# Kernel optimization log

Hardware: AMD Instinct MI355X
Metric: run time of the kernel (lower is better)

## Reference

```python
import jax, jax.numpy as jnp
import numpy as np

B, S, D, H = 2, 2048, 2048, 16
HD = D // H
RESIDUAL_SCALE = 1.0
EPS = 1e-6


def setup_inputs() -> dict:
    key = jax.random.key(0)
    ks = jax.random.split(key, 6)
    x = jax.random.normal(ks[0], (B, S, D), jnp.float32)
    # rotary tables: emb = cat(freqs, freqs), shape [S, HD]
    inv_freq = 1.0 / (10000.0 ** (jnp.arange(0, HD, 2, dtype=jnp.float32) / HD))
    t = jnp.arange(S, dtype=jnp.float32)
    freqs = jnp.einsum('s,f->sf', t, inv_freq)
    emb = jnp.concatenate([freqs, freqs], axis=-1)
    cos, sin = jnp.cos(emb), jnp.sin(emb)
    sc = 0.02
    w_qkv = jax.random.normal(ks[1], (3 * D, D), jnp.float32) * sc
    w_out = jax.random.normal(ks[2], (D, D), jnp.float32) * sc
    w_fc1 = jax.random.normal(ks[3], (4 * D, D), jnp.float32) * sc
    w_fc2 = jax.random.normal(ks[4], (D, 4 * D), jnp.float32) * sc
    g1 = jnp.ones((D,), jnp.float32)
    g2 = jnp.ones((D,), jnp.float32)
    return {'x': x, 'cos': cos, 'sin': sin, 'g1': g1, 'g2': g2,
            'w_qkv': w_qkv, 'w_out': w_out, 'w_fc1': w_fc1, 'w_fc2': w_fc2}


def _rmsnorm(x, g):
    xf = x.astype(jnp.float32)
    norm = jnp.sqrt(jnp.mean(xf * xf, axis=-1, keepdims=True) + EPS)
    return g * (xf / norm)


def _rotate_half(x):
    x1, x2 = jnp.split(x, 2, axis=-1)
    return jnp.concatenate([-x2, x1], axis=-1)


def _rope(t, cos, sin):
    # t: [B, S, H, HD]; cos/sin: [S, HD]
    c = cos[None, :, None, :]
    s = sin[None, :, None, :]
    return t * c + _rotate_half(t) * s


def reference(x, cos, sin, g1, g2, w_qkv, w_out, w_fc1, w_fc2):
    b, s, d = x.shape
    x_skip = x
    h = _rmsnorm(x, g1)
    qkv = (h @ w_qkv.T).reshape(b, s, 3, H, HD)
    q = _rope(qkv[:, :, 0], cos, sin)
    k = _rope(qkv[:, :, 1], cos, sin)
    v = qkv[:, :, 2]  # rotary is identity on v
    scale = 1.0 / jnp.sqrt(jnp.asarray(HD, dtype=q.dtype))
    scores = jnp.einsum('bqhd,bkhd->bhqk', q, k) * scale
    causal = jnp.triu(jnp.ones((s, s), dtype=bool), k=1)
    scores = jnp.where(causal[None, None], -jnp.inf, scores)
    attn = jax.nn.softmax(scores, axis=-1)
    o = jnp.einsum('bhqk,bkhd->bqhd', attn, v).reshape(b, s, d)
    x = x_skip + RESIDUAL_SCALE * (o @ w_out.T)
    x_skip = x
    h = _rmsnorm(x, g2)
    h = jax.nn.gelu(h @ w_fc1.T, approximate=True) @ w_fc2.T
    return x_skip + RESIDUAL_SCALE * h
```

## Files before the change

kernel.cpp:

```cpp
#include <hip/hip_runtime.h>
#include <stdint.h>

typedef unsigned short u16;
typedef u16 u16x4 __attribute__((ext_vector_type(4)));
typedef u16 u16x8 __attribute__((ext_vector_type(8)));
typedef __bf16 bf16x8 __attribute__((ext_vector_type(8)));
typedef float f32x4 __attribute__((ext_vector_type(4)));
typedef float f32x16 __attribute__((ext_vector_type(16)));

#define MFMA16 __builtin_amdgcn_mfma_f32_16x16x32_bf16
#define MFMA32 __builtin_amdgcn_mfma_f32_32x32x16_bf16

static __device__ __forceinline__ float b2f(u16 u) {
    union { unsigned int i; float f; } v; v.i = ((unsigned int)u) << 16; return v.f;
}
static __device__ __forceinline__ u16 f2b(float f) {
    union { float f; unsigned int i; } v; v.f = f;
    unsigned int r = (v.i + 0x7fffu + ((v.i >> 16) & 1u)) >> 16;
    return (u16)r;
}
static __device__ __forceinline__ unsigned pk2(float lo, float hi) {
    union { __bf16 b[2]; unsigned u; } t;
    t.b[0] = (__bf16)lo; t.b[1] = (__bf16)hi; return t.u;
}
static __device__ __forceinline__ void gload_lds16(const void* g, void* l) {
    __builtin_amdgcn_global_load_lds((__attribute__((address_space(1))) void*)g,
                                     (__attribute__((address_space(3))) void*)l,
                                     16, 0, 0);
}

__global__ __launch_bounds__(256) void cvt_k(const float* __restrict__ in,
                                             u16* __restrict__ out, long n) {
    long i = ((long)blockIdx.x * 256 + threadIdx.x) * 4;
    if (i >= n) return;
    float4 v = *(const float4*)(in + i);
    u16x4 o; o[0] = f2b(v.x); o[1] = f2b(v.y); o[2] = f2b(v.z); o[3] = f2b(v.w);
    *(u16x4*)(out + i) = o;
}

__global__ __launch_bounds__(256) void addred_k(float* __restrict__ xout,
                                                const float* __restrict__ p0,
                                                const float* __restrict__ p1) {
    long i = ((long)blockIdx.x * 256 + threadIdx.x) * 4;
    float4 a = *(const float4*)(xout + i);
    float4 b = *(const float4*)(p0 + i);
    float4 c = *(const float4*)(p1 + i);
    a.x += b.x + c.x; a.y += b.y + c.y; a.z += b.z + c.z; a.w += b.w + c.w;
    *(float4*)(xout + i) = a;
}

__global__ __launch_bounds__(256) void addrednorm_k(float* xout,
                                                    const float* __restrict__ x,
                                                    const float* p0,
                                                    const float* __restrict__ p1,
                                                    const float* __restrict__ g,
                                                    u16* __restrict__ out) {
    const long row = blockIdx.x;
    const int tid = threadIdx.x;
    const long base = row * 2048;
    float4 a = *(const float4*)(x + base + tid * 4);
    float4 b = *(const float4*)(p0 + base + tid * 4);
    float4 c = *(const float4*)(p1 + base + tid * 4);
    a.x += b.x + c.x; a.y += b.y + c.y; a.z += b.z + c.z; a.w += b.w + c.w;
    float4 a2 = *(const float4*)(x + base + 1024 + tid * 4);
    float4 b2 = *(const float4*)(p0 + base + 1024 + tid * 4);
    float4 c2 = *(const float4*)(p1 + base + 1024 + tid * 4);
    a2.x += b2.x + c2.x; a2.y += b2.y + c2.y;
    a2.z += b2.z + c2.z; a2.w += b2.w + c2.w;
    *(float4*)(xout + base + tid * 4) = a;
    *(float4*)(xout + base + 1024 + tid * 4) = a2;
    float ss = a.x*a.x + a.y*a.y + a.z*a.z + a.w*a.w
             + a2.x*a2.x + a2.y*a2.y + a2.z*a2.z + a2.w*a2.w;
    #pragma unroll
    for (int d = 1; d < 64; d <<= 1) ss += __shfl_xor(ss, d);
    __shared__ float red[4];
    if ((tid & 63) == 0) red[tid >> 6] = ss;
    __syncthreads();
    float tot = red[0] + red[1] + red[2] + red[3];
    float rinv = rsqrtf(tot * (1.0f / 2048.0f) + 1e-6f);
    float4 g0 = *(const float4*)(g + tid * 4);
    float4 g1 = *(const float4*)(g + 1024 + tid * 4);
    u16x4 o0, o1;
    o0[0] = f2b(a.x * g0.x * rinv); o0[1] = f2b(a.y * g0.y * rinv);
    o0[2] = f2b(a.z * g0.z * rinv); o0[3] = f2b(a.w * g0.w * rinv);
    o1[0] = f2b(a2.x * g1.x * rinv); o1[1] = f2b(a2.y * g1.y * rinv);
    o1[2] = f2b(a2.z * g1.z * rinv); o1[3] = f2b(a2.w * g1.w * rinv);
    *(u16x4*)(out + base + tid * 4) = o0;
    *(u16x4*)(out + base + 1024 + tid * 4) = o1;
}

__global__ __launch_bounds__(256) void rmsnorm_k(const float* __restrict__ x,
                                                 const float* __restrict__ g,
                                                 u16* __restrict__ out) {
    const long row = blockIdx.x;
    const int tid = threadIdx.x;
    const float* xr = x + row * 2048;
    float4 a = *(const float4*)(xr + tid * 4);
    float4 b = *(const float4*)(xr + 1024 + tid * 4);
    float ss = a.x*a.x + a.y*a.y + a.z*a.z + a.w*a.w
             + b.x*b.x + b.y*b.y + b.z*b.z + b.w*b.w;
    #pragma unroll
    for (int d = 1; d < 64; d <<= 1) ss += __shfl_xor(ss, d);
    __shared__ float red[4];
    if ((tid & 63) == 0) red[tid >> 6] = ss;
    __syncthreads();
    float tot = red[0] + red[1] + red[2] + red[3];
    float rinv = rsqrtf(tot * (1.0f / 2048.0f) + 1e-6f);
    float4 g0 = *(const float4*)(g + tid * 4);
    float4 g1 = *(const float4*)(g + 1024 + tid * 4);
    u16x4 o0, o1;
    o0[0] = f2b(a.x * g0.x * rinv); o0[1] = f2b(a.y * g0.y * rinv);
    o0[2] = f2b(a.z * g0.z * rinv); o0[3] = f2b(a.w * g0.w * rinv);
    o1[0] = f2b(b.x * g1.x * rinv); o1[1] = f2b(b.y * g1.y * rinv);
    o1[2] = f2b(b.z * g1.z * rinv); o1[3] = f2b(b.w * g1.w * rinv);
    *(u16x4*)(out + row * 2048 + tid * 4) = o0;
    *(u16x4*)(out + row * 2048 + 1024 + tid * 4) = o1;
}

__global__ __launch_bounds__(256) void rope_k(u16* __restrict__ qkv,
                                              const float* __restrict__ cosb,
                                              const float* __restrict__ sinb) {
    long idx = (long)blockIdx.x * 256 + threadIdx.x;
    int d = (int)(idx & 15) * 4;
    int h = (int)((idx >> 4) & 15);
    int which = (int)((idx >> 8) & 1);
    long row = idx >> 9;
    int s = (int)(row & 2047);
    u16* base = qkv + row * 6144 + which * 2048 + h * 128;
    u16x4 ua = *(u16x4*)(base + d);
    u16x4 ub = *(u16x4*)(base + d + 64);
    float4 c4 = *(const float4*)(cosb + (long)s * 128 + d);
    float4 s4 = *(const float4*)(sinb + (long)s * 128 + d);
    float cc[4] = {c4.x, c4.y, c4.z, c4.w};
    float sn[4] = {s4.x, s4.y, s4.z, s4.w};
    float scale = (which == 0) ? 0.08838834764831845f : 1.0f;
    u16x4 oa, ob;
    #pragma unroll
    for (int j = 0; j < 4; ++j) {
        float a = b2f(ua[j]), b = b2f(ub[j]);
        oa[j] = f2b((a * cc[j] - b * sn[j]) * scale);
        ob[j] = f2b((b * cc[j] + a * sn[j]) * scale);
    }
    *(u16x4*)(base + d) = oa;
    *(u16x4*)(base + d + 64) = ob;
}

#define DS_A(BUF, SM, KK) (*(const bf16x8*)(ldsb + (BUF)*32768 + \
        ((((SM)*2) + (KK)) << 10) + rin64 + cst2))
#define DS_B(BUF, SN, KK) (*(const bf16x8*)(ldsb + 65536 + (BUF)*32768 + \
        ((((SN)*2) + (KK)) << 10) + rin64 + cst2))
#define STAGE_AB(BUF, SK, KT) do { \
    gload_lds16(sA0 + ((long)(KT)*64 + (SK)*32), ldsb + (BUF)*32768 + (w4 + (SK))*1024); \
    gload_lds16(sA1 + ((long)(KT)*64 + (SK)*32), ldsb + (BUF)*32768 + (w4 + 2 + (SK))*1024); \
    gload_lds16(sB0 + ((long)(KT)*64 + (SK)*32), ldsb + 65536 + (BUF)*32768 + (w4 + (SK))*1024); \
    gload_lds16(sB1 + ((long)(KT)*64 + (SK)*32), ldsb + 65536 + (BUF)*32768 + (w4 + 2 + (SK))*1024); \
} while (0)
#define PHASE(BUF, MH, KK, RDB, STAGE_STMT, VM) do { \
    bf16x8 af[4]; \
    _Pragma("unroll") \
    for (int m = 0; m < 4; ++m) af[m] = DS_A(BUF, wr8 + (MH)*4 + m, KK); \
    if (RDB) { \
        bfr[0] = DS_B(BUF, wc4 + 0, KK); bfr[1] = DS_B(BUF, wc4 + 1, KK); \
        bfr[2] = DS_B(BUF, wc4 + 2, KK); bfr[3] = DS_B(BUF, wc4 + 3, KK); \
    } \
    STAGE_STMT; \
    if (VM) { asm volatile("s_waitcnt vmcnt(8)" ::: "memory"); } \
    __builtin_amdgcn_sched_barrier(0); \
    __builtin_amdgcn_s_barrier(); \
    __builtin_amdgcn_sched_barrier(0); \
    __builtin_amdgcn_s_setprio(1); \
    _Pragma("unroll") \
    for (int m = 0; m < 4; ++m) \
        _Pragma("unroll") \
        for (int n = 0; n < 4; ++n) \
            acc[(MH)*4 + m][n] = MFMA16(af[m], bfr[n], acc[(MH)*4 + m][n], 0, 0, 0); \
    __builtin_amdgcn_s_setprio(0); \
    __builtin_amdgcn_sched_barrier(0); \
    __builtin_amdgcn_s_barrier(); \
    __builtin_amdgcn_sched_barrier(0); \
} while (0)

template <int EPI>
__global__ __launch_bounds__(512, 2) void gemm256(const u16* __restrict__ A,
                                                  const u16* __restrict__ W,
                                                  int M, int N, int K,
                                                  u16* outb, float* outf,
                                                  float* outf2, const float* res,
                                                  u16* vtw, int ksplit) {
    __shared__ u16 lds_[65536];
    char* ldsb = (char*)lds_;
    const int tid = threadIdx.x;
    const int w = tid >> 6, l = tid & 63;
    const int w4 = w * 4;
    const int wr8 = (w >> 2) * 8;
    const int wc4 = (w & 3) * 4;
    const int rin64 = (l & 15) * 64;
    const int cst2 = ((((l >> 4) * 8) ^ (((l >> 3) & 1) << 4)) << 1);

    const int nbn = N >> 8;
    const int nbm = M >> 8;
    const int nwg = gridDim.x;
    const int cpx = nwg >> 3;
    const int bid = blockIdx.x;
    int wg = (bid & 7) * cpx + (bid >> 3);
    int kseg = 0;
    int Keff = K;
    if (ksplit == 2) {
        kseg = wg & 1;
        wg >>= 1;
        Keff = K >> 1;
    }
    const int grp = 8 * nbn;
    const int g8 = wg / grp;
    const int rem = wg - g8 * grp;
    const int bm0 = g8 * 8;
    const int gmh = (nbm - bm0 < 8) ? (nbm - bm0) : 8;
    const int bn = rem / gmh;
    const int bm = bm0 + rem % gmh;
    const u16* Ab = A + (long)kseg * Keff;
    const u16* Wb = W + (long)kseg * Keff;

    const int r4 = l >> 2;
    const int clog = ((l & 3) * 8) ^ (((r4 >> 3) & 1) << 4);
    const u16* sA0 = Ab + ((long)bm * 256 + (w * 2 + 0) * 16 + r4) * K + clog;
    const u16* sA1 = Ab + ((long)bm * 256 + (w * 2 + 1) * 16 + r4) * K + clog;
    const u16* sB0 = Wb + ((long)bn * 256 + (w * 2 + 0) * 16 + r4) * K + clog;
    const u16* sB1 = Wb + ((long)bn * 256 + (w * 2 + 1) * 16 + r4) * K + clog;

    f32x4 acc[8][4];
    #pragma unroll
    for (int m = 0; m < 8; ++m)
        #pragma unroll
        for (int n = 0; n < 4; ++n) acc[m][n] = (f32x4){0.f, 0.f, 0.f, 0.f};
    bf16x8 bfr[4];

    const int nkt = Keff >> 6;
    const int niter = nkt >> 1;

    STAGE_AB(0, 0, 0); STAGE_AB(0, 1, 0); STAGE_AB(1, 0, 1);
    asm volatile("s_waitcnt vmcnt(8)" ::: "memory");
    __builtin_amdgcn_sched_barrier(0);
    __builtin_amdgcn_s_barrier();
    __builtin_amdgcn_sched_barrier(0);

    for (int it = 0; it < niter; ++it) {
        const int t = it * 2;
        const int t1 = t + 1;
        const int t2 = (t + 2 < nkt) ? t + 2 : nkt - 1;
        const int t3 = (t + 3 < nkt) ? t + 3 : nkt - 1;
        PHASE(0, 0, 0, 1, STAGE_AB(1, 1, t1), 0);
        PHASE(0, 1, 0, 0, ;, 1);
        PHASE(0, 0, 1, 1, STAGE_AB(0, 0, t2), 0);
        PHASE(0, 1, 1, 0, ;, 1);
        PHASE(1, 0, 0, 1, STAGE_AB(0, 1, t2), 0);
        PHASE(1, 1, 0, 0, ;, 1);
        PHASE(1, 0, 1, 1, STAGE_AB(1, 0, t3), 0);
        PHASE(1, 1, 1, 0, ;, 1);
    }
    asm volatile("s_waitcnt vmcnt(0)" ::: "memory");

    const int rb = bm * 256 + (wr8 >> 3) * 128 + ((l >> 4) << 2);
    const int cb = bn * 256 + (w & 3) * 64 + (l & 15);
    if (EPI == 4) {
        const bool vreg = (cb >= 4096);
        #pragma unroll
        for (int m = 0; m < 8; ++m) {
            long row0 = rb + m * 16;
            #pragma unroll
            for (int n = 0; n < 4; ++n) {
                long col = cb + n * 16;
                if (vreg) {
                    int d = (int)col & 127;
                    int hh = ((int)col >> 7) - 32;
                    long bh = (row0 >> 11) * 16 + hh;
                    int s = (int)(row0 & 2047);
                    u16x4 o4;
                    #pragma unroll
                    for (int r = 0; r < 4; ++r) o4[r] = f2b(acc[m][n][r]);
                    *(u16x4*)(vtw + (bh * 128 + d) * 2048 + s) = o4;
                } else {
                    #pragma unroll
                    for (int r = 0; r < 4; ++r)
                        outb[(row0 + r) * N + col] = f2b(acc[m][n][r]);
                }
            }
        }
        return;
    }
    float* pf = (EPI == 3) ? (kseg ? outf2 : outf) : outf;
    #pragma unroll
    for (int m = 0; m < 8; ++m) {
        #pragma unroll
        for (int r = 0; r < 4; ++r) {
            long row = rb + m * 16 + r;
            #pragma unroll
            for (int n = 0; n < 4; ++n) {
                long col = cb + n * 16;
                float v = acc[m][n][r];
                if (EPI == 1) {
                    pf[row * N + col] = res[row * N + col] + v;
                } else if (EPI == 2) {
                    float u = 0.7978845608028654f * v * (1.0f + 0.044715f * v * v);
                    float e = __expf(2.0f * u);
                    float tgl = 1.0f - 2.0f / (e + 1.0f);
                    outb[row * N + col] = f2b(0.5f * v * (1.0f + tgl));
                } else if (EPI == 3) {
                    pf[row * N + col] = v;
                } else {
                    outb[row * N + col] = f2b(v);
                }
            }
        }
    }
}

struct AttnState {
    f32x16 acc[4];
    float m_i, l_i;
};

template <bool DIAG>
static __device__ __forceinline__ void attn_tile(
    int kv0, int qg, bool do_g1, int l31, int hi,
    const u16* __restrict__ Ks, const u16* __restrict__ Vt,
    const bf16x8 (&qf)[8], AttnState& st)
{
    f32x16 sacc0, sacc1;
    #pragma unroll
    for (int r = 0; r < 16; ++r) { sacc0[r] = 0.f; sacc1[r] = 0.f; }

    #pragma unroll
    for (int dsl = 0; dsl < 8; ++dsl) {
        int slot = dsl * 2 + hi;
        int kv = l31;
        int sw = (slot & 8) | ((slot & 7) ^ (kv & 7));
        bf16x8 kf = *(const bf16x8*)(Ks + kv * 128 + sw * 8);
        sacc0 = MFMA32(kf, qf[dsl], sacc0, 0, 0, 0);
    }
    if (do_g1) {
        #pragma unroll
        for (int dsl = 0; dsl < 8; ++dsl) {
            int slot = dsl * 2 + hi;
            int kv = 32 + l31;
            int sw = (slot & 8) | ((slot & 7) ^ (kv & 7));
            bf16x8 kf = *(const bf16x8*)(Ks + kv * 128 + sw * 8);
            sacc1 = MFMA32(kf, qf[dsl], sacc1, 0, 0, 0);
        }
    }

    float sv[2][16];
    #pragma unroll
    for (int r = 0; r < 16; ++r) {
        sv[0][r] = sacc0[r];
        sv[1][r] = do_g1 ? sacc1[r] : -INFINITY;
    }
    if (DIAG) {
        #pragma unroll
        for (int g = 0; g < 2; ++g)
            #pragma unroll
            for (int r = 0; r < 16; ++r) {
                int kvg = kv0 + g * 32 + ((r & 3) + 8 * (r >> 2) + 4 * hi);
                if (kvg > qg) sv[g][r] = -INFINITY;
            }
    }

    float mx = sv[0][0];
    #pragma unroll
    for (int r = 1; r < 16; ++r) mx = fmaxf(mx, sv[0][r]);
    #pragma unroll
    for (int r = 0; r < 16; ++r) mx = fmaxf(mx, sv[1][r]);
    mx = fmaxf(mx, __shfl_xor(mx, 32));

    bool defer = __all(mx <= st.m_i + 8.0f);
    if (!defer) {
        float mnew = fmaxf(st.m_i, mx);
        float f = __expf(st.m_i - mnew);
        st.l_i *= f;
        #pragma unroll
        for (int dblk = 0; dblk < 4; ++dblk)
            #pragma unroll
            for (int r = 0; r < 16; ++r) st.acc[dblk][r] *= f;
        st.m_i = mnew;
    }

    float ssum = 0.f;
    #pragma unroll
    for (int g = 0; g < 2; ++g)
        #pragma unroll
        for (int r = 0; r < 16; ++r) {
            float e = __expf(sv[g][r] - st.m_i);
            sv[g][r] = e;
            ssum += e;
        }
    ssum += __shfl_xor(ssum, 32);
    st.l_i += ssum;

    unsigned w[2][4][2];
    #pragma unroll
    for (int g = 0; g < 2; ++g)
        #pragma unroll
        for (int q4 = 0; q4 < 4; ++q4) {
            w[g][q4][0] = pk2(sv[g][4 * q4 + 0], sv[g][4 * q4 + 1]);
            w[g][q4][1] = pk2(sv[g][4 * q4 + 2], sv[g][4 * q4 + 3]);
        }
    bf16x8 pfrag[4];
    #pragma unroll
    for (int ks = 0; ks < 4; ++ks) {
        int g = ks >> 1, h2 = ks & 1;
        unsigned o0 = hi ? w[g][2 * h2 + 1][0] : w[g][2 * h2][0];
        unsigned o1 = hi ? w[g][2 * h2 + 1][1] : w[g][2 * h2][1];
        unsigned t0 = hi ? w[g][2 * h2][0] : w[g][2 * h2 + 1][0];
        unsigned t1 = hi ? w[g][2 * h2][1] : w[g][2 * h2 + 1][1];
        unsigned s0v = __shfl_xor(t0, 32);
        unsigned s1v = __shfl_xor(t1, 32);
        union { unsigned u[4]; bf16x8 v; } cv;
        cv.u[0] = hi ? s0v : o0;
        cv.u[1] = hi ? s1v : o1;
        cv.u[2] = hi ? o0 : s0v;
        cv.u[3] = hi ? o1 : s1v;
        pfrag[ks] = cv.v;
    }

    #pragma unroll
    for (int dblk = 0; dblk < 4; ++dblk) {
        int d = dblk * 32 + l31;
        #pragma unroll
        for (int ks = 0; ks < 4; ++ks) {
            if (ks >= 2 && !do_g1) continue;
            int slot = ks * 2 + hi;
            bf16x8 vf = *(const bf16x8*)(Vt + d * 64 + (slot ^ (d & 7)) * 8);
            st.acc[dblk] = MFMA32(vf, pfrag[ks], st.acc[dblk], 0, 0, 0);
        }
    }
}

__global__ __launch_bounds__(256) void attn3_k(const u16* __restrict__ qkv,
                                               const u16* __restrict__ vt,
                                               u16* __restrict__ out) {
    const int bh = blockIdx.y;
    const int b = bh >> 4, h = bh & 15;
    const int qb = blockIdx.x;
    const int q0 = qb * 128;
    const int tid = threadIdx.x, wave = tid >> 6, lane = tid & 63;
    const int l31 = lane & 31, hi = lane >> 5;
    const int brow = b * 2048;
    __shared__ u16 Ks_lds[2][64 * 128];
    __shared__ u16 Vt_lds[2][128 * 64];

    const int krow = tid >> 4;
    const int kslot = tid & 15;
    const int vrow = tid >> 3;
    const int vslot = tid & 7;

    bf16x8 qf[8];
    {
        const u16* qp = qkv + (long)(brow + q0 + wave * 32 + l31) * 6144 +
                        h * 128 + hi * 8;
        #pragma unroll
        for (int dsl = 0; dsl < 8; ++dsl) qf[dsl] = *(const bf16x8*)(qp + dsl * 16);
    }

    AttnState st;
    st.m_i = -INFINITY; st.l_i = 0.f;
    #pragma unroll
    for (int dblk = 0; dblk < 4; ++dblk)
        #pragma unroll
        for (int r = 0; r < 16; ++r) st.acc[dblk][r] = 0.f;

    const int r0 = q0 + wave * 32;
    const int qg = r0 + l31;
    const int nt = 2 * qb + 2;
    int cur = 0;

#define STAGE_KV(BUF, KV0) do { \
    _Pragma("unroll") \
    for (int i = 0; i < 4; ++i) { \
        int kv = i * 16 + krow; \
        int sw = (kslot & 8) | ((kslot & 7) ^ (kv & 7)); \
        const u16* src = qkv + (long)(brow + (KV0) + kv) * 6144 + 2048 + \
                         h * 128 + sw * 8; \
        gload_lds16(src, (char*)Ks_lds[BUF] + (i * 16 + wave * 4) * 256); \
    } \
    _Pragma("unroll") \
    for (int i = 0; i < 4; ++i) { \
        int d = i * 32 + vrow; \
        int sw = vslot ^ (d & 7); \
        const u16* src = vt + ((long)bh * 128 + d) * 2048 + (KV0) + sw * 8; \
        gload_lds16(src, (char*)Vt_lds[BUF] + (i * 32 + wave * 8) * 128); \
    } \
} while (0)

    STAGE_KV(0, 0);
    for (int t = 0; t < nt; ++t) {
        const int kv0 = t * 64;
        const bool more = (t + 1 < nt);
        if (more) {
            if (cur) STAGE_KV(0, kv0 + 64); else STAGE_KV(1, kv0 + 64);
        }
        if (more) { asm volatile("s_waitcnt vmcnt(8)" ::: "memory"); }
        else      { asm volatile("s_waitcnt vmcnt(0)" ::: "memory"); }
        __builtin_amdgcn_sched_barrier(0);
        __builtin_amdgcn_s_barrier();
        __builtin_amdgcn_sched_barrier(0);
        {
            const u16* Ks = Ks_lds[cur];
            const u16* Vt_ = Vt_lds[cur];
            const int delta = r0 - kv0;
            if (delta >= 64)
                attn_tile<false>(kv0, qg, true, l31, hi, Ks, Vt_, qf, st);
            else if (delta >= 0)
                attn_tile<true>(kv0, qg, delta >= 32, l31, hi, Ks, Vt_, qf, st);
        }
        __builtin_amdgcn_sched_barrier(0);
        __builtin_amdgcn_s_barrier();
        __builtin_amdgcn_sched_barrier(0);
        cur ^= 1;
    }
#undef STAGE_KV

    float inv = 1.0f / st.l_i;
    long orow = (long)(brow + q0 + wave * 32 + l31);
    #pragma unroll
    for (int dblk = 0; dblk < 4; ++dblk)
        #pragma unroll
        for (int rq = 0; rq < 4; ++rq) {
            u16x4 o4;
            #pragma unroll
            for (int m = 0; m < 4; ++m) o4[m] = f2b(st.acc[dblk][rq * 4 + m] * inv);
            int d = dblk * 32 + 8 * rq + 4 * hi;
            *(u16x4*)(out + orow * 2048 + h * 128 + d) = o4;
        }
}

extern "C" void kernel_launch(void* const* d_in, const int* in_sizes, int n_in,
                              void* d_out, int out_size, void* d_ws, size_t ws_size,
                              hipStream_t stream) {
    const float* x     = (const float*)d_in[0];
    const float* cosb  = (const float*)d_in[1];
    const float* sinb  = (const float*)d_in[2];
    const float* g1    = (const float*)d_in[3];
    const float* g2    = (const float*)d_in[4];
    const float* w_qkv = (const float*)d_in[5];
    const float* w_out = (const float*)d_in[6];
    const float* w_fc1 = (const float*)d_in[7];
    const float* w_fc2 = (const float*)d_in[8];

    char* ws = (char*)d_ws;
    u16* wqkv_b = (u16*)(ws);
    u16* wout_b = (u16*)(ws + 25165824);
    u16* wfc1_b = (u16*)(ws + 33554432);
    u16* wfc2_b = (u16*)(ws + 67108864);
    u16* h_b    = (u16*)(ws + 100663296);
    u16* qkv_b  = (u16*)(ws + 117440512);
    u16* attn_b = (u16*)(ws + 167772160);
    u16* hg_b   = qkv_b;
    u16* vt_b   = (u16*)d_out;
    float* p0op = (float*)d_out;
    float* p1op = (float*)(ws + 117440512);
    float* part = (float*)ws;
    float* xout = (float*)d_out;

    cvt_k<<<12288, 256, 0, stream>>>(w_qkv, wqkv_b, 12582912L);
    cvt_k<<<4096, 256, 0, stream>>>(w_out, wout_b, 4194304L);
    cvt_k<<<16384, 256, 0, stream>>>(w_fc1, wfc1_b, 16777216L);
    cvt_k<<<16384, 256, 0, stream>>>(w_fc2, wfc2_b, 16777216L);

    rmsnorm_k<<<4096, 256, 0, stream>>>(x, g1, h_b);
    gemm256<4><<<384, 512, 0, stream>>>(h_b, wqkv_b, 4096, 6144, 2048,
                                        qkv_b, nullptr, nullptr, nullptr,
                                        vt_b, 1);
    rope_k<<<8192, 256, 0, stream>>>(qkv_b, cosb, sinb);
    attn3_k<<<dim3(16, 32), 256, 0, stream>>>(qkv_b, vt_b, attn_b);
    gemm256<3><<<256, 512, 0, stream>>>(attn_b, wout_b, 4096, 2048, 2048,
                                        nullptr, p0op, p1op, nullptr,
                                        nullptr, 2);
    addrednorm_k<<<4096, 256, 0, stream>>>(xout, x, p0op, p1op, g2, h_b);
    gemm256<2><<<512, 512, 0, stream>>>(h_b, wfc1_b, 4096, 8192, 2048,
                                        hg_b, nullptr, nullptr, nullptr,
                                        nullptr, 1);
    gemm256<3><<<256, 512, 0, stream>>>(hg_b, wfc2_b, 4096, 2048, 8192,
                                        nullptr, part, part + 8388608, nullptr,
                                        nullptr, 2);
    addred_k<<<8192, 256, 0, stream>>>(xout, part, part + 8388608);
}
```

Measured before the change: 618.0 us.

## Split GEMM A/B staging across phases and raise wave priority around attention MFMAs

The GEMM main loop now issues A and B global-to-LDS loads as separate half-stages, one per phase, instead of issuing all four loads together every other phase. The vmcnt waits are retuned to match (6/8/10) so each buffer is drained just before it is read. The goal is to spread memory issue evenly across the MFMA phases and overlap it better. The attention tile also wraps its QK and PV MFMA loops in s_setprio(1) to favour matrix work over softmax and shuffle work in other waves. Wrong vmcnt values could cause stale LDS reads or stalls that cost more than they save.

```diff
diff --git a/kernel.cpp b/kernel.cpp
--- a/kernel.cpp
+++ b/kernel.cpp
@@ -149,13 +149,15 @@
         ((((SM)*2) + (KK)) << 10) + rin64 + cst2))
 #define DS_B(BUF, SN, KK) (*(const bf16x8*)(ldsb + 65536 + (BUF)*32768 + \
         ((((SN)*2) + (KK)) << 10) + rin64 + cst2))
-#define STAGE_AB(BUF, SK, KT) do { \
+#define STAGE_A(BUF, SK, KT) do { \
     gload_lds16(sA0 + ((long)(KT)*64 + (SK)*32), ldsb + (BUF)*32768 + (w4 + (SK))*1024); \
     gload_lds16(sA1 + ((long)(KT)*64 + (SK)*32), ldsb + (BUF)*32768 + (w4 + 2 + (SK))*1024); \
+} while (0)
+#define STAGE_B(BUF, SK, KT) do { \
     gload_lds16(sB0 + ((long)(KT)*64 + (SK)*32), ldsb + 65536 + (BUF)*32768 + (w4 + (SK))*1024); \
     gload_lds16(sB1 + ((long)(KT)*64 + (SK)*32), ldsb + 65536 + (BUF)*32768 + (w4 + 2 + (SK))*1024); \
 } while (0)
-#define PHASE(BUF, MH, KK, RDB, STAGE_STMT, VM) do { \
+#define PHASE(BUF, MH, KK, RDB, STAGE_STMT, DRAIN_STMT) do { \
     bf16x8 af[4]; \
     _Pragma("unroll") \
     for (int m = 0; m < 4; ++m) af[m] = DS_A(BUF, wr8 + (MH)*4 + m, KK); \
@@ -164,7 +166,7 @@
         bfr[2] = DS_B(BUF, wc4 + 2, KK); bfr[3] = DS_B(BUF, wc4 + 3, KK); \
     } \
     STAGE_STMT; \
-    if (VM) { asm volatile("s_waitcnt vmcnt(8)" ::: "memory"); } \
+    DRAIN_STMT; \
     __builtin_amdgcn_sched_barrier(0); \
     __builtin_amdgcn_s_barrier(); \
     __builtin_amdgcn_sched_barrier(0); \
@@ -179,6 +181,9 @@
     __builtin_amdgcn_s_barrier(); \
     __builtin_amdgcn_sched_barrier(0); \
 } while (0)
+#define VM6  asm volatile("s_waitcnt vmcnt(6)" ::: "memory")
+#define VM8  asm volatile("s_waitcnt vmcnt(8)" ::: "memory")
+#define VM10 asm volatile("s_waitcnt vmcnt(10)" ::: "memory")
 
 template <int EPI>
 __global__ __launch_bounds__(512, 2) void gemm256(const u16* __restrict__ A,
@@ -237,8 +242,9 @@
     const int nkt = Keff >> 6;
     const int niter = nkt >> 1;
 
-    STAGE_AB(0, 0, 0); STAGE_AB(0, 1, 0); STAGE_AB(1, 0, 1);
-    asm volatile("s_waitcnt vmcnt(8)" ::: "memory");
+    STAGE_B(0, 0, 0); STAGE_A(0, 0, 0); STAGE_B(0, 1, 0); STAGE_A(0, 1, 0);
+    STAGE_B(1, 0, 1); STAGE_A(1, 0, 1); STAGE_B(1, 1, 1);
+    VM6;
     __builtin_amdgcn_sched_barrier(0);
     __builtin_amdgcn_s_barrier();
     __builtin_amdgcn_sched_barrier(0);
@@ -248,14 +254,14 @@
         const int t1 = t + 1;
         const int t2 = (t + 2 < nkt) ? t + 2 : nkt - 1;
         const int t3 = (t + 3 < nkt) ? t + 3 : nkt - 1;
-        PHASE(0, 0, 0, 1, STAGE_AB(1, 1, t1), 0);
-        PHASE(0, 1, 0, 0, ;, 1);
-        PHASE(0, 0, 1, 1, STAGE_AB(0, 0, t2), 0);
-        PHASE(0, 1, 1, 0, ;, 1);
-        PHASE(1, 0, 0, 1, STAGE_AB(0, 1, t2), 0);
-        PHASE(1, 1, 0, 0, ;, 1);
-        PHASE(1, 0, 1, 1, STAGE_AB(1, 0, t3), 0);
-        PHASE(1, 1, 1, 0, ;, 1);
+        PHASE(0, 0, 0, 1, STAGE_A(1, 1, t1), ;);
+        PHASE(0, 1, 0, 0, STAGE_B(0, 0, t2), ;);
+        PHASE(0, 0, 1, 1, STAGE_A(0, 0, t2), ;);
+        PHASE(0, 1, 1, 0, STAGE_B(0, 1, t2), VM8);
+        PHASE(1, 0, 0, 1, STAGE_A(0, 1, t2), ;);
+        PHASE(1, 1, 0, 0, STAGE_B(1, 0, t3), VM10);
+        PHASE(1, 0, 1, 1, STAGE_A(1, 0, t3), ;);
+        PHASE(1, 1, 1, 0, STAGE_B(1, 1, t3), VM6);
     }
     asm volatile("s_waitcnt vmcnt(0)" ::: "memory");
 
@@ -329,6 +335,7 @@
     #pragma unroll
     for (int r = 0; r < 16; ++r) { sacc0[r] = 0.f; sacc1[r] = 0.f; }
 
+    __builtin_amdgcn_s_setprio(1);
     #pragma unroll
     for (int dsl = 0; dsl < 8; ++dsl) {
         int slot = dsl * 2 + hi;
@@ -347,6 +354,7 @@
             sacc1 = MFMA32(kf, qf[dsl], sacc1, 0, 0, 0);
         }
     }
+    __builtin_amdgcn_s_setprio(0);
 
     float sv[2][16];
     #pragma unroll
@@ -421,6 +429,7 @@
         pfrag[ks] = cv.v;
     }
 
+    __builtin_amdgcn_s_setprio(1);
     #pragma unroll
     for (int dblk = 0; dblk < 4; ++dblk) {
         int d = dblk * 32 + l31;
@@ -432,6 +441,7 @@
             st.acc[dblk] = MFMA32(vf, pfrag[ks], st.acc[dblk], 0, 0, 0);
         }
     }
+    __builtin_amdgcn_s_setprio(0);
 }
 
 __global__ __launch_bounds__(256) void attn3_k(const u16* __restrict__ qkv,
```

Result: faster. 597.5 us (-3.3%).
